# Optimization experiments

Hardware: AMD Instinct MI355X
Metric: run time of the kernel (lower is better)

Reference implementation:

```python
import jax, jax.numpy as jnp
import numpy as np

NUM_CLASS = 32
ALPHA = 1.0
GAMMA = 2.0
EPS = 1e-8  # torch F.cosine_similarity norm clamp


def setup_inputs() -> dict:
    key = jax.random.key(0)
    k1, k2 = jax.random.split(key)
    B, D, W, H, C = 8, 256, 160, 160, NUM_CLASS
    decod_feature = jax.random.normal(k1, (B, D, W, H), dtype=jnp.float32)
    mask = (jax.random.uniform(k2, (B, C, W, H)) < 0.05).astype(jnp.float32)
    return {"decod_feature": decod_feature, "mask": mask}


def reference(decod_feature, mask):
    # Per class c: gather feature vectors f_i (dim D) at pixels where mask==1,
    # sum cosine_similarity(f_i, f_j) over i<j, divide by n(n+1)/2.
    # With unit-normalized u_i: sum_{i<j} u_i.u_j = (||sum_i u_i||^2 - n) / 2.
    norms = jnp.sqrt(jnp.sum(decod_feature * decod_feature, axis=1, keepdims=True))
    U = decod_feature / jnp.maximum(norms, EPS)          # [B,D,W,H] normalized pixel features
    s = jnp.einsum('bdwh,bcwh->cd', U, mask)             # [C,D] per-class sum of unit vectors
    n = jnp.sum(mask, axis=(0, 2, 3))                    # [C] pixels per class
    pair_sum = (jnp.sum(s * s, axis=1) - n) * 0.5        # sum over i<j of cos sims
    denom = n * (n + 1.0) * 0.5
    class_loss = jnp.where(n > 0, pair_sum / jnp.maximum(denom, 1.0), 0.0)
    emb_loss = jnp.sum(class_loss) / NUM_CLASS
    return ALPHA * jnp.exp(-GAMMA * emb_loss)
```

## Files before the change

### kernel.cpp

```cpp
#include <hip/hip_runtime.h>
#include <hip/hip_bf16.h>
#include <cstdint>
#include <cstddef>

#define NUM_CLASS 32
#define D_DIM 256
#define PIX_PER_IMG 25600
#define TILE_PX 64
#define TILES_PER_IMG 400
#define N_TILES 3200
#define BLOCK_THREADS 512
#define MAX_GRID 256

typedef __attribute__((ext_vector_type(4))) float  f32x4;
typedef __attribute__((ext_vector_type(8))) __bf16 bf16x8;
typedef unsigned short ushort8 __attribute__((ext_vector_type(8)));

__device__ __forceinline__ unsigned short f2bf(float x) {
    unsigned u = __builtin_bit_cast(unsigned, x);
    unsigned r = (u + 0x7fffu + ((u >> 16) & 1u)) >> 16;
    return (unsigned short)r;
}

__device__ __forceinline__ ushort8 pack_bf8(f32x4 a, f32x4 b) {
    ushort8 r;
    r[0] = f2bf(a.x); r[1] = f2bf(a.y); r[2] = f2bf(a.z); r[3] = f2bf(a.w);
    r[4] = f2bf(b.x); r[5] = f2bf(b.y); r[6] = f2bf(b.z); r[7] = f2bf(b.w);
    return r;
}

__device__ __forceinline__ void gll16(const float* src, float* ldst) {
    __builtin_amdgcn_global_load_lds(
        (const __attribute__((address_space(1))) float*)src,
        (__attribute__((address_space(3))) float*)ldst, 16, 0, 0);
}

#define SWZROW(base, row, g) \
    (*(const f32x4*)((const char*)(base) + (row) * 256 + ((((g) ^ (((row) & 7) << 1))) << 4)))

__global__ __launch_bounds__(BLOCK_THREADS)
void emb_main(const float* __restrict__ feat, const float* __restrict__ mask,
              float* __restrict__ part, float* __restrict__ npart, int G)
{
    __shared__ __align__(16) float ftile[2][D_DIM][TILE_PX];
    __shared__ __align__(16) float mtile[2][NUM_CLASS][TILE_PX];
    __shared__ __align__(16) float ssq_s[8][TILE_PX];
    __shared__ __align__(16) unsigned short inv_bf[TILE_PX];

    const int t = threadIdx.x;
    const int lane = t & 63;
    const int wave = t >> 6;
    const int blk  = blockIdx.x;
    const int lh = lane >> 4;
    const int ll = lane & 15;

    const int nt = (blk < N_TILES) ? ((N_TILES - 1 - blk) / G + 1) : 0;

    f32x4 acc[2][2] = {};
    float ncA = 0.f, ncB = 0.f;

    auto stage = [&](int ti, int buf) {
        const int b  = ti / TILES_PER_IMG;
        const int p0 = (ti - b * TILES_PER_IMG) * TILE_PX;
        const float* fb = feat + (size_t)b * ((size_t)D_DIM * PIX_PER_IMG) + p0;
        #pragma unroll
        for (int j = 0; j < 8; ++j) {
            const int dr = wave * 32 + j * 4;
            const int d  = dr + lh;
            const int g  = ll ^ ((d & 7) << 1);
            gll16(fb + (size_t)d * PIX_PER_IMG + g * 4, &ftile[buf][dr][0]);
        }
        const int c  = wave * 4 + lh;
        const int gm = ll ^ ((c & 7) << 1);
        gll16(mask + (size_t)b * (NUM_CLASS * PIX_PER_IMG) + (size_t)c * PIX_PER_IMG + p0 + gm * 4,
              &mtile[buf][wave * 4][0]);
    };

    if (nt > 0) stage(blk, 0);

    const int rg   = wave * 4 + lh;
    const int soff = ((ll ^ ((rg & 7) << 1)) << 4);

    for (int i = 0; i < nt; ++i) {
        const int buf = i & 1;
        if (i + 1 < nt) {
            stage(blk + (i + 1) * G, buf ^ 1);
            asm volatile("s_waitcnt vmcnt(9)" ::: "memory");
        } else {
            asm volatile("s_waitcnt vmcnt(0)" ::: "memory");
        }
        __builtin_amdgcn_s_barrier();
        __builtin_amdgcn_sched_barrier(0);

        const char* fbase = (const char*)&ftile[buf][0][0];
        f32x4 ss = {0.f, 0.f, 0.f, 0.f};
        #pragma unroll
        for (int k = 0; k < 8; ++k) {
            const int d = rg + 32 * k;
            const f32x4 v = *(const f32x4*)(fbase + d * 256 + soff);
            ss += v * v;
        }
        ss.x += __shfl_down(ss.x, 32); ss.y += __shfl_down(ss.y, 32);
        ss.z += __shfl_down(ss.z, 32); ss.w += __shfl_down(ss.w, 32);
        ss.x += __shfl_down(ss.x, 16); ss.y += __shfl_down(ss.y, 16);
        ss.z += __shfl_down(ss.z, 16); ss.w += __shfl_down(ss.w, 16);
        if (lane < 16) *(f32x4*)&ssq_s[wave][lane * 4] = ss;
        __builtin_amdgcn_sched_barrier(0);
        asm volatile("s_waitcnt lgkmcnt(0)" ::: "memory");
        __builtin_amdgcn_s_barrier();
        __builtin_amdgcn_sched_barrier(0);

        if (t < TILE_PX) {
            float tot = 0.f;
            #pragma unroll
            for (int w = 0; w < 8; ++w) tot += ssq_s[w][t];
            inv_bf[t] = f2bf(1.0f / fmaxf(sqrtf(tot), 1e-8f));
        }
        __builtin_amdgcn_sched_barrier(0);
        asm volatile("s_waitcnt lgkmcnt(0)" ::: "memory");
        __builtin_amdgcn_s_barrier();
        __builtin_amdgcn_sched_barrier(0);

        const char* mbase = (const char*)&mtile[buf][0][0];
        const int dbase = wave * 32;
        #pragma unroll
        for (int ks = 0; ks < 2; ++ks) {
            const int kp0 = ks * 32 + lh * 8;
            const int g0  = kp0 >> 2;
            const ushort8 iv = *(const ushort8*)(inv_bf + kp0);

            const f32x4 ma0 = SWZROW(mbase, ll,      g0);
            const f32x4 ma1 = SWZROW(mbase, ll,      g0 + 1);
            const f32x4 mb0 = SWZROW(mbase, 16 + ll, g0);
            const f32x4 mb1 = SWZROW(mbase, 16 + ll, g0 + 1);
            ushort8 a0, a1;
            #pragma unroll
            for (int q = 0; q < 4; ++q) {
                a0[q]     = (ma0[q] > 0.5f) ? iv[q]     : (unsigned short)0;
                a0[q + 4] = (ma1[q] > 0.5f) ? iv[q + 4] : (unsigned short)0;
                a1[q]     = (mb0[q] > 0.5f) ? iv[q]     : (unsigned short)0;
                a1[q + 4] = (mb1[q] > 0.5f) ? iv[q + 4] : (unsigned short)0;
            }
            if (wave == 0) {
                ncA += ma0[0] + ma0[1] + ma0[2] + ma0[3] + ma1[0] + ma1[1] + ma1[2] + ma1[3];
                ncB += mb0[0] + mb0[1] + mb0[2] + mb0[3] + mb1[0] + mb1[1] + mb1[2] + mb1[3];
            }

            const f32x4 f00 = SWZROW(fbase, dbase + ll,      g0);
            const f32x4 f01 = SWZROW(fbase, dbase + ll,      g0 + 1);
            const f32x4 f10 = SWZROW(fbase, dbase + 16 + ll, g0);
            const f32x4 f11 = SWZROW(fbase, dbase + 16 + ll, g0 + 1);

            const bf16x8 ba0 = __builtin_bit_cast(bf16x8, a0);
            const bf16x8 ba1 = __builtin_bit_cast(bf16x8, a1);
            const bf16x8 bb0 = __builtin_bit_cast(bf16x8, pack_bf8(f00, f01));
            const bf16x8 bb1 = __builtin_bit_cast(bf16x8, pack_bf8(f10, f11));

            acc[0][0] = __builtin_amdgcn_mfma_f32_16x16x32_bf16(ba0, bb0, acc[0][0], 0, 0, 0);
            acc[0][1] = __builtin_amdgcn_mfma_f32_16x16x32_bf16(ba0, bb1, acc[0][1], 0, 0, 0);
            acc[1][0] = __builtin_amdgcn_mfma_f32_16x16x32_bf16(ba1, bb0, acc[1][0], 0, 0, 0);
            acc[1][1] = __builtin_amdgcn_mfma_f32_16x16x32_bf16(ba1, bb1, acc[1][1], 0, 0, 0);
        }
        __builtin_amdgcn_sched_barrier(0);
        asm volatile("s_waitcnt lgkmcnt(0)" ::: "memory");
        __builtin_amdgcn_s_barrier();
        __builtin_amdgcn_sched_barrier(0);
    }

    {
        float* myout = part + (size_t)blk * (NUM_CLASS * D_DIM);
        const int dbase = wave * 32;
        #pragma unroll
        for (int mt = 0; mt < 2; ++mt)
            #pragma unroll
            for (int ntile = 0; ntile < 2; ++ntile)
                #pragma unroll
                for (int r = 0; r < 4; ++r) {
                    const int c = mt * 16 + lh * 4 + r;
                    const int d = dbase + ntile * 16 + ll;
                    myout[c * D_DIM + d] = acc[mt][ntile][r];
                }
    }
    ncA += __shfl_xor(ncA, 16); ncA += __shfl_xor(ncA, 32);
    ncB += __shfl_xor(ncB, 16); ncB += __shfl_xor(ncB, 32);
    if (wave == 0 && lane < 16) {
        npart[(size_t)blk * NUM_CLASS + lane]      = ncA;
        npart[(size_t)blk * NUM_CLASS + 16 + lane] = ncB;
    }
}

__global__ __launch_bounds__(1024)
void emb_reduce(const float* __restrict__ part, const float* __restrict__ npart,
                float* __restrict__ cls, int G)
{
    const int c = blockIdx.x;
    const int t = threadIdx.x;
    const int d = t & 255, gs = t >> 8;
    float s = 0.f;
    #pragma unroll 8
    for (int g = gs; g < G; g += 4)
        s += part[(size_t)g * (NUM_CLASS * D_DIM) + c * D_DIM + d];
    __shared__ float red[4][256];
    red[gs][d] = s;
    float nsum = 0.f;
    for (int g = t; g < G; g += 1024) nsum += npart[(size_t)g * NUM_CLASS + c];
    __syncthreads();
    float s2 = 0.f;
    if (t < 256) {
        const float tot = red[0][t] + red[1][t] + red[2][t] + red[3][t];
        s2 = tot * tot;
    }
    const int lane = t & 63, wave = t >> 6;
    #pragma unroll
    for (int off = 32; off > 0; off >>= 1) {
        s2   += __shfl_down(s2, off);
        nsum += __shfl_down(nsum, off);
    }
    __shared__ float rs[16], rn[16];
    if (lane == 0) { rs[wave] = s2; rn[wave] = nsum; }
    __syncthreads();
    if (t == 0) {
        float S2 = 0.f, N = 0.f;
        #pragma unroll
        for (int w = 0; w < 16; ++w) { S2 += rs[w]; N += rn[w]; }
        const float pair = 0.5f * (S2 - N);
        const float den  = 0.5f * N * (N + 1.0f);
        cls[c] = (N > 0.f) ? (pair / fmaxf(den, 1.0f)) : 0.f;
    }
}

__global__ void emb_final(const float* __restrict__ cls, float* __restrict__ out)
{
    const int t = threadIdx.x;
    float v = (t < NUM_CLASS) ? cls[t] : 0.f;
    #pragma unroll
    for (int off = 32; off > 0; off >>= 1) v += __shfl_down(v, off);
    if (t == 0) {
        const float emb = v / (float)NUM_CLASS;
        out[0] = 1.0f * expf(-2.0f * emb);
    }
}

extern "C" void kernel_launch(void* const* d_in, const int* in_sizes, int n_in,
                              void* d_out, int out_size, void* d_ws, size_t ws_size,
                              hipStream_t stream)
{
    const float* feat = (const float*)d_in[0];
    const float* mask = (const float*)d_in[1];
    float* out = (float*)d_out;

    const size_t per_blk = (size_t)(NUM_CLASS * D_DIM + NUM_CLASS) * sizeof(float);
    int G = MAX_GRID;
    size_t need = (size_t)G * per_blk + NUM_CLASS * sizeof(float);
    if (ws_size < need) {
        size_t g = (ws_size > NUM_CLASS * sizeof(float))
                       ? (ws_size - NUM_CLASS * sizeof(float)) / per_blk : 1;
        if (g < 1) g = 1;
        if (g > MAX_GRID) g = MAX_GRID;
        G = (int)g;
    }
    float* part  = (float*)d_ws;
    float* npart = part + (size_t)G * (NUM_CLASS * D_DIM);
    float* cls   = npart + (size_t)G * NUM_CLASS;

    emb_main<<<G, BLOCK_THREADS, 0, stream>>>(feat, mask, part, npart, G);
    emb_reduce<<<NUM_CLASS, 1024, 0, stream>>>(part, npart, cls, G);
    emb_final<<<1, 64, 0, stream>>>(cls, out);
}
```

Before: 52.31 us.

## Replace per-block partials and reduce kernels with atomics and last-block finalize

Each block now atomically adds its class-by-dim sums and class counts into one global accumulator instead of writing per-block partials. A global counter picks the last block, which computes the per-class loss and the final scalar, so the separate reduce and final kernels go away. This cuts two kernel launches and the partial-buffer traffic, but adds a memset, heavy float atomic contention on an 8K-element array, and nondeterministic summation order.

Result: slower. 86.29 us (+64.9%).

```diff
diff --git a/kernel.cpp b/kernel.cpp
--- a/kernel.cpp
+++ b/kernel.cpp
@@ -40,12 +40,15 @@
 
 __global__ __launch_bounds__(BLOCK_THREADS)
 void emb_main(const float* __restrict__ feat, const float* __restrict__ mask,
-              float* __restrict__ part, float* __restrict__ npart, int G)
+              float* __restrict__ sacc, float* __restrict__ nacc,
+              unsigned int* __restrict__ ctr, float* __restrict__ out, int G)
 {
     __shared__ __align__(16) float ftile[2][D_DIM][TILE_PX];
     __shared__ __align__(16) float mtile[2][NUM_CLASS][TILE_PX];
     __shared__ __align__(16) float ssq_s[8][TILE_PX];
     __shared__ __align__(16) unsigned short inv_bf[TILE_PX];
+    __shared__ unsigned int winner;
+    __shared__ float clsv[NUM_CLASS];
 
     const int t = threadIdx.x;
     const int lane = t & 63;
@@ -168,7 +171,6 @@
     }
 
     {
-        float* myout = part + (size_t)blk * (NUM_CLASS * D_DIM);
         const int dbase = wave * 32;
         #pragma unroll
         for (int mt = 0; mt < 2; ++mt)
@@ -178,66 +180,50 @@
                 for (int r = 0; r < 4; ++r) {
                     const int c = mt * 16 + lh * 4 + r;
                     const int d = dbase + ntile * 16 + ll;
-                    myout[c * D_DIM + d] = acc[mt][ntile][r];
+                    unsafeAtomicAdd(&sacc[c * D_DIM + d], acc[mt][ntile][r]);
                 }
     }
     ncA += __shfl_xor(ncA, 16); ncA += __shfl_xor(ncA, 32);
     ncB += __shfl_xor(ncB, 16); ncB += __shfl_xor(ncB, 32);
     if (wave == 0 && lane < 16) {
-        npart[(size_t)blk * NUM_CLASS + lane]      = ncA;
-        npart[(size_t)blk * NUM_CLASS + 16 + lane] = ncB;
-    }
-}
-
-__global__ __launch_bounds__(1024)
-void emb_reduce(const float* __restrict__ part, const float* __restrict__ npart,
-                float* __restrict__ cls, int G)
-{
-    const int c = blockIdx.x;
-    const int t = threadIdx.x;
-    const int d = t & 255, gs = t >> 8;
-    float s = 0.f;
-    #pragma unroll 8
-    for (int g = gs; g < G; g += 4)
-        s += part[(size_t)g * (NUM_CLASS * D_DIM) + c * D_DIM + d];
-    __shared__ float red[4][256];
-    red[gs][d] = s;
-    float nsum = 0.f;
-    for (int g = t; g < G; g += 1024) nsum += npart[(size_t)g * NUM_CLASS + c];
+        unsafeAtomicAdd(&nacc[lane],      ncA);
+        unsafeAtomicAdd(&nacc[16 + lane], ncB);
+    }
+
+    __threadfence();
+    if (t == 0) winner = atomicAdd(ctr, 1u);
     __syncthreads();
-    float s2 = 0.f;
+    if (winner != (unsigned)(G - 1)) return;
+    __threadfence();
+
+    float p2 = 0.f;
     if (t < 256) {
-        const float tot = red[0][t] + red[1][t] + red[2][t] + red[3][t];
-        s2 = tot * tot;
-    }
-    const int lane = t & 63, wave = t >> 6;
-    #pragma unroll
-    for (int off = 32; off > 0; off >>= 1) {
-        s2   += __shfl_down(s2, off);
-        nsum += __shfl_down(nsum, off);
-    }
-    __shared__ float rs[16], rn[16];
-    if (lane == 0) { rs[wave] = s2; rn[wave] = nsum; }
+        const int c = t >> 3, j = t & 7;
+        const int base = c * D_DIM + j * 32;
+        #pragma unroll 8
+        for (int q = 0; q < 32; ++q) {
+            const float v = __hip_atomic_load(&sacc[base + q], __ATOMIC_RELAXED,
+                                              __HIP_MEMORY_SCOPE_AGENT);
+            p2 += v * v;
+        }
+    }
+    p2 += __shfl_down(p2, 4);
+    p2 += __shfl_down(p2, 2);
+    p2 += __shfl_down(p2, 1);
+    if (t < 256 && (t & 7) == 0) {
+        const int c = t >> 3;
+        const float N = __hip_atomic_load(&nacc[c], __ATOMIC_RELAXED,
+                                          __HIP_MEMORY_SCOPE_AGENT);
+        const float pair = 0.5f * (p2 - N);
+        const float den  = 0.5f * N * (N + 1.0f);
+        clsv[c] = (N > 0.f) ? (pair / fmaxf(den, 1.0f)) : 0.f;
+    }
     __syncthreads();
-    if (t == 0) {
-        float S2 = 0.f, N = 0.f;
-        #pragma unroll
-        for (int w = 0; w < 16; ++w) { S2 += rs[w]; N += rn[w]; }
-        const float pair = 0.5f * (S2 - N);
-        const float den  = 0.5f * N * (N + 1.0f);
-        cls[c] = (N > 0.f) ? (pair / fmaxf(den, 1.0f)) : 0.f;
-    }
-}
-
-__global__ void emb_final(const float* __restrict__ cls, float* __restrict__ out)
-{
-    const int t = threadIdx.x;
-    float v = (t < NUM_CLASS) ? cls[t] : 0.f;
-    #pragma unroll
-    for (int off = 32; off > 0; off >>= 1) v += __shfl_down(v, off);
-    if (t == 0) {
-        const float emb = v / (float)NUM_CLASS;
-        out[0] = 1.0f * expf(-2.0f * emb);
+    if (t < 32) {
+        float v = clsv[t];
+        #pragma unroll
+        for (int off = 16; off; off >>= 1) v += __shfl_down(v, off);
+        if (t == 0) out[0] = expf(-2.0f * (v / (float)NUM_CLASS));
     }
 }
 
@@ -249,21 +235,14 @@
     const float* mask = (const float*)d_in[1];
     float* out = (float*)d_out;
 
-    const size_t per_blk = (size_t)(NUM_CLASS * D_DIM + NUM_CLASS) * sizeof(float);
-    int G = MAX_GRID;
-    size_t need = (size_t)G * per_blk + NUM_CLASS * sizeof(float);
-    if (ws_size < need) {
-        size_t g = (ws_size > NUM_CLASS * sizeof(float))
-                       ? (ws_size - NUM_CLASS * sizeof(float)) / per_blk : 1;
-        if (g < 1) g = 1;
-        if (g > MAX_GRID) g = MAX_GRID;
-        G = (int)g;
-    }
-    float* part  = (float*)d_ws;
-    float* npart = part + (size_t)G * (NUM_CLASS * D_DIM);
-    float* cls   = npart + (size_t)G * NUM_CLASS;
-
-    emb_main<<<G, BLOCK_THREADS, 0, stream>>>(feat, mask, part, npart, G);
-    emb_reduce<<<NUM_CLASS, 1024, 0, stream>>>(part, npart, cls, G);
-    emb_final<<<1, 64, 0, stream>>>(cls, out);
-}
+    float* sacc = (float*)d_ws;
+    float* nacc = sacc + NUM_CLASS * D_DIM;
+    unsigned int* ctr = (unsigned int*)(nacc + NUM_CLASS);
+    const size_t zbytes = (size_t)(NUM_CLASS * D_DIM + NUM_CLASS) * sizeof(float)
+                        + sizeof(unsigned int);
+
+    hipMemsetAsync(d_ws, 0, zbytes, stream);
+
+    const int G = MAX_GRID;
+    emb_main<<<G, BLOCK_THREADS, 0, stream>>>(feat, mask, sacc, nacc, ctr, out, G);
+}
```

## Load tiles into registers and stage bf16 copies in LDS instead of fp32 async loads

Applied to the files above, without the earlier changes.

Replaces the double-buffered fp32 global_load_lds staging with register prefetch of the next tile. Each wave converts its features and masks to bf16 (via v_cvt_pk_bf16_f32) and stores them into a single swizzled bf16 LDS tile. This cuts LDS footprint by about 4x, allowing a launch bound of 4 blocks per CU, removes the repeated fp32-to-bf16 packing in the MFMA loop, and drops one barrier. In exchange it relies on register-held prefetch for latency hiding and removes the LDS double buffer, which could expose load latency or raise register pressure.

Result: faster. 50.20 us (-4.0%).

```diff
diff --git a/kernel.cpp b/kernel.cpp
--- a/kernel.cpp
+++ b/kernel.cpp
@@ -15,6 +15,7 @@
 typedef __attribute__((ext_vector_type(4))) float  f32x4;
 typedef __attribute__((ext_vector_type(8))) __bf16 bf16x8;
 typedef unsigned short ushort8 __attribute__((ext_vector_type(8)));
+typedef unsigned int   uint2v  __attribute__((ext_vector_type(2)));
 
 __device__ __forceinline__ unsigned short f2bf(float x) {
     unsigned u = __builtin_bit_cast(unsigned, x);
@@ -22,28 +23,25 @@
     return (unsigned short)r;
 }
 
-__device__ __forceinline__ ushort8 pack_bf8(f32x4 a, f32x4 b) {
-    ushort8 r;
-    r[0] = f2bf(a.x); r[1] = f2bf(a.y); r[2] = f2bf(a.z); r[3] = f2bf(a.w);
-    r[4] = f2bf(b.x); r[5] = f2bf(b.y); r[6] = f2bf(b.z); r[7] = f2bf(b.w);
+__device__ __forceinline__ unsigned cvt_pk_bf16(float lo, float hi) {
+    unsigned r;
+    asm("v_cvt_pk_bf16_f32 %0, %1, %2" : "=v"(r) : "v"(lo), "v"(hi));
     return r;
 }
 
-__device__ __forceinline__ void gll16(const float* src, float* ldst) {
-    __builtin_amdgcn_global_load_lds(
-        (const __attribute__((address_space(1))) float*)src,
-        (__attribute__((address_space(3))) float*)ldst, 16, 0, 0);
-}
-
-#define SWZROW(base, row, g) \
-    (*(const f32x4*)((const char*)(base) + (row) * 256 + ((((g) ^ (((row) & 7) << 1))) << 4)))
-
-__global__ __launch_bounds__(BLOCK_THREADS)
+__device__ __forceinline__ int bt_w(int row, int p4) {
+    return row * 128 + ((((p4 >> 1) ^ (row & 7)) << 4)) + ((p4 & 1) << 3);
+}
+__device__ __forceinline__ int bt_r(int row, int j) {
+    return row * 128 + (((j ^ (row & 7)) << 4));
+}
+
+__global__ __launch_bounds__(BLOCK_THREADS, 4)
 void emb_main(const float* __restrict__ feat, const float* __restrict__ mask,
               float* __restrict__ part, float* __restrict__ npart, int G)
 {
-    __shared__ __align__(16) float ftile[2][D_DIM][TILE_PX];
-    __shared__ __align__(16) float mtile[2][NUM_CLASS][TILE_PX];
+    __shared__ __align__(16) unsigned char ftb[D_DIM * 128];
+    __shared__ __align__(16) unsigned char mtb[NUM_CLASS * 128];
     __shared__ __align__(16) float ssq_s[8][TILE_PX];
     __shared__ __align__(16) unsigned short inv_bf[TILE_PX];
 
@@ -53,58 +51,61 @@
     const int blk  = blockIdx.x;
     const int lh = lane >> 4;
     const int ll = lane & 15;
+    const int mc  = t >> 4;
+    const int mpg = t & 15;
 
     const int nt = (blk < N_TILES) ? ((N_TILES - 1 - blk) / G + 1) : 0;
 
     f32x4 acc[2][2] = {};
-    float ncA = 0.f, ncB = 0.f;
-
-    auto stage = [&](int ti, int buf) {
+    float nc = 0.f;
+
+    f32x4 fv[8];
+    f32x4 mv;
+
+    auto issue = [&](int ti) {
         const int b  = ti / TILES_PER_IMG;
         const int p0 = (ti - b * TILES_PER_IMG) * TILE_PX;
-        const float* fb = feat + (size_t)b * ((size_t)D_DIM * PIX_PER_IMG) + p0;
-        #pragma unroll
-        for (int j = 0; j < 8; ++j) {
-            const int dr = wave * 32 + j * 4;
-            const int d  = dr + lh;
-            const int g  = ll ^ ((d & 7) << 1);
-            gll16(fb + (size_t)d * PIX_PER_IMG + g * 4, &ftile[buf][dr][0]);
-        }
-        const int c  = wave * 4 + lh;
-        const int gm = ll ^ ((c & 7) << 1);
-        gll16(mask + (size_t)b * (NUM_CLASS * PIX_PER_IMG) + (size_t)c * PIX_PER_IMG + p0 + gm * 4,
-              &mtile[buf][wave * 4][0]);
+        const float* fb = feat + (size_t)b * ((size_t)D_DIM * PIX_PER_IMG) + p0 + ll * 4;
+        #pragma unroll
+        for (int k = 0; k < 8; ++k) {
+            const int d = wave * 4 + lh + 32 * k;
+            fv[k] = *(const f32x4*)(fb + (size_t)d * PIX_PER_IMG);
+        }
+        mv = *(const f32x4*)(mask + (size_t)b * (NUM_CLASS * PIX_PER_IMG)
+                             + (size_t)mc * PIX_PER_IMG + p0 + mpg * 4);
     };
 
-    if (nt > 0) stage(blk, 0);
-
-    const int rg   = wave * 4 + lh;
-    const int soff = ((ll ^ ((rg & 7) << 1)) << 4);
+    if (nt > 0) issue(blk);
 
     for (int i = 0; i < nt; ++i) {
-        const int buf = i & 1;
-        if (i + 1 < nt) {
-            stage(blk + (i + 1) * G, buf ^ 1);
-            asm volatile("s_waitcnt vmcnt(9)" ::: "memory");
-        } else {
-            asm volatile("s_waitcnt vmcnt(0)" ::: "memory");
-        }
         __builtin_amdgcn_s_barrier();
         __builtin_amdgcn_sched_barrier(0);
 
-        const char* fbase = (const char*)&ftile[buf][0][0];
         f32x4 ss = {0.f, 0.f, 0.f, 0.f};
         #pragma unroll
         for (int k = 0; k < 8; ++k) {
-            const int d = rg + 32 * k;
-            const f32x4 v = *(const f32x4*)(fbase + d * 256 + soff);
-            ss += v * v;
+            const int d = wave * 4 + lh + 32 * k;
+            ss += fv[k] * fv[k];
+            uint2v w;
+            w.x = cvt_pk_bf16(fv[k].x, fv[k].y);
+            w.y = cvt_pk_bf16(fv[k].z, fv[k].w);
+            *(uint2v*)(ftb + bt_w(d, ll)) = w;
+        }
+        nc += mv.x + mv.y + mv.z + mv.w;
+        {
+            uint2v w;
+            w.x = cvt_pk_bf16(mv.x, mv.y);
+            w.y = cvt_pk_bf16(mv.z, mv.w);
+            *(uint2v*)(mtb + bt_w(mc, mpg)) = w;
         }
         ss.x += __shfl_down(ss.x, 32); ss.y += __shfl_down(ss.y, 32);
         ss.z += __shfl_down(ss.z, 32); ss.w += __shfl_down(ss.w, 32);
         ss.x += __shfl_down(ss.x, 16); ss.y += __shfl_down(ss.y, 16);
         ss.z += __shfl_down(ss.z, 16); ss.w += __shfl_down(ss.w, 16);
         if (lane < 16) *(f32x4*)&ssq_s[wave][lane * 4] = ss;
+
+        if (i + 1 < nt) issue(blk + (i + 1) * G);
+
         __builtin_amdgcn_sched_barrier(0);
         asm volatile("s_waitcnt lgkmcnt(0)" ::: "memory");
         __builtin_amdgcn_s_barrier();
@@ -121,72 +122,53 @@
         __builtin_amdgcn_s_barrier();
         __builtin_amdgcn_sched_barrier(0);
 
-        const char* mbase = (const char*)&mtile[buf][0][0];
         const int dbase = wave * 32;
         #pragma unroll
         for (int ks = 0; ks < 2; ++ks) {
-            const int kp0 = ks * 32 + lh * 8;
-            const int g0  = kp0 >> 2;
-            const ushort8 iv = *(const ushort8*)(inv_bf + kp0);
-
-            const f32x4 ma0 = SWZROW(mbase, ll,      g0);
-            const f32x4 ma1 = SWZROW(mbase, ll,      g0 + 1);
-            const f32x4 mb0 = SWZROW(mbase, 16 + ll, g0);
-            const f32x4 mb1 = SWZROW(mbase, 16 + ll, g0 + 1);
+            const int j   = ks * 4 + lh;
+            const int kp0 = j * 8;
+            const ushort8 iv = *(const ushort8*)((const char*)inv_bf + kp0 * 2);
+            const ushort8 m0 = *(const ushort8*)(mtb + bt_r(ll,      j));
+            const ushort8 m1 = *(const ushort8*)(mtb + bt_r(16 + ll, j));
+            const ushort8 b0 = *(const ushort8*)(ftb + bt_r(dbase + ll,      j));
+            const ushort8 b1 = *(const ushort8*)(ftb + bt_r(dbase + 16 + ll, j));
             ushort8 a0, a1;
             #pragma unroll
-            for (int q = 0; q < 4; ++q) {
-                a0[q]     = (ma0[q] > 0.5f) ? iv[q]     : (unsigned short)0;
-                a0[q + 4] = (ma1[q] > 0.5f) ? iv[q + 4] : (unsigned short)0;
-                a1[q]     = (mb0[q] > 0.5f) ? iv[q]     : (unsigned short)0;
-                a1[q + 4] = (mb1[q] > 0.5f) ? iv[q + 4] : (unsigned short)0;
+            for (int q = 0; q < 8; ++q) {
+                a0[q] = m0[q] ? iv[q] : (unsigned short)0;
+                a1[q] = m1[q] ? iv[q] : (unsigned short)0;
             }
-            if (wave == 0) {
-                ncA += ma0[0] + ma0[1] + ma0[2] + ma0[3] + ma1[0] + ma1[1] + ma1[2] + ma1[3];
-                ncB += mb0[0] + mb0[1] + mb0[2] + mb0[3] + mb1[0] + mb1[1] + mb1[2] + mb1[3];
-            }
-
-            const f32x4 f00 = SWZROW(fbase, dbase + ll,      g0);
-            const f32x4 f01 = SWZROW(fbase, dbase + ll,      g0 + 1);
-            const f32x4 f10 = SWZROW(fbase, dbase + 16 + ll, g0);
-            const f32x4 f11 = SWZROW(fbase, dbase + 16 + ll, g0 + 1);
-
             const bf16x8 ba0 = __builtin_bit_cast(bf16x8, a0);
             const bf16x8 ba1 = __builtin_bit_cast(bf16x8, a1);
-            const bf16x8 bb0 = __builtin_bit_cast(bf16x8, pack_bf8(f00, f01));
-            const bf16x8 bb1 = __builtin_bit_cast(bf16x8, pack_bf8(f10, f11));
-
+            const bf16x8 bb0 = __builtin_bit_cast(bf16x8, b0);
+            const bf16x8 bb1 = __builtin_bit_cast(bf16x8, b1);
             acc[0][0] = __builtin_amdgcn_mfma_f32_16x16x32_bf16(ba0, bb0, acc[0][0], 0, 0, 0);
             acc[0][1] = __builtin_amdgcn_mfma_f32_16x16x32_bf16(ba0, bb1, acc[0][1], 0, 0, 0);
             acc[1][0] = __builtin_amdgcn_mfma_f32_16x16x32_bf16(ba1, bb0, acc[1][0], 0, 0, 0);
             acc[1][1] = __builtin_amdgcn_mfma_f32_16x16x32_bf16(ba1, bb1, acc[1][1], 0, 0, 0);
         }
         __builtin_amdgcn_sched_barrier(0);
-        asm volatile("s_waitcnt lgkmcnt(0)" ::: "memory");
-        __builtin_amdgcn_s_barrier();
-        __builtin_amdgcn_sched_barrier(0);
     }
 
     {
         float* myout = part + (size_t)blk * (NUM_CLASS * D_DIM);
         const int dbase = wave * 32;
         #pragma unroll
-        for (int mt = 0; mt < 2; ++mt)
+        for (int m = 0; m < 2; ++m)
             #pragma unroll
-            for (int ntile = 0; ntile < 2; ++ntile)
+            for (int n = 0; n < 2; ++n)
                 #pragma unroll
                 for (int r = 0; r < 4; ++r) {
-                    const int c = mt * 16 + lh * 4 + r;
-                    const int d = dbase + ntile * 16 + ll;
-                    myout[c * D_DIM + d] = acc[mt][ntile][r];
+                    const int c = m * 16 + lh * 4 + r;
+                    const int d = dbase + n * 16 + ll;
+                    myout[c * D_DIM + d] = acc[m][n][r];
                 }
     }
-    ncA += __shfl_xor(ncA, 16); ncA += __shfl_xor(ncA, 32);
-    ncB += __shfl_xor(ncB, 16); ncB += __shfl_xor(ncB, 32);
-    if (wave == 0 && lane < 16) {
-        npart[(size_t)blk * NUM_CLASS + lane]      = ncA;
-        npart[(size_t)blk * NUM_CLASS + 16 + lane] = ncB;
-    }
+    nc += __shfl_down(nc, 8);
+    nc += __shfl_down(nc, 4);
+    nc += __shfl_down(nc, 2);
+    nc += __shfl_down(nc, 1);
+    if (mpg == 0) npart[(size_t)blk * NUM_CLASS + mc] = nc;
 }
 
 __global__ __launch_bounds__(1024)
```
